# Kernel optimization log

Measured on AMD Instinct MI355X. Metric: run time of the kernel, lower is better.

Reference implementation:

```python
import jax, jax.numpy as jnp
import numpy as np

B, L, HID, NH = 8, 1024, 1024, 16
DH = HID // NH
EPS = 1e-12


def _linear(x, W, b):
    # torch nn.Linear: y = x @ W.T + b
    return jnp.einsum('ble,oe->blo', x, W) + b


def _attend(qx, kx, vx, mask, Wq, bq, Wk, bk, Wv, bv):
    q = _linear(qx, Wq, bq).reshape(B, -1, NH, DH)
    k = _linear(kx, Wk, bk).reshape(B, -1, NH, DH)
    v = _linear(vx, Wv, bv).reshape(B, -1, NH, DH)
    scores = jnp.einsum('bqhd,bkhd->bhqk', q, k) / np.sqrt(DH).astype(np.float32)
    scores = scores + mask  # additive mask broadcast [B,1,1,Lk]
    probs = jax.nn.softmax(scores, axis=-1)  # dropout = identity (eval mode)
    ctx = jnp.einsum('bhqk,bkhd->bqhd', probs, v)
    return ctx.reshape(B, -1, HID)


def _layernorm(x, gamma, beta):
    mu = jnp.mean(x, axis=-1, keepdims=True)
    var = jnp.mean(jnp.square(x - mu), axis=-1, keepdims=True)
    return gamma * (x - mu) * jax.lax.rsqrt(var + EPS) + beta


def setup_inputs():
    key = jax.random.key(0)
    ks = jax.random.split(key, 20)
    s = 0.02
    d = {
        'cinput_tensor': jax.random.normal(ks[0], (B, L, HID), jnp.float32),
        'qinput_tensor': jax.random.normal(ks[1], (B, L, HID), jnp.float32),
        'attention_mask': jnp.zeros((B, 1, 1, L), jnp.float32),
        'qattention_mask': jnp.zeros((B, 1, 1, L), jnp.float32),
    }
    names = ['Wq', 'Wk', 'Wv', 'Wqq', 'Wqk', 'Wqv', 'Wo']
    for i, n in enumerate(names):
        d[n] = jax.random.normal(ks[2 + i], (HID, HID), jnp.float32) * s
        d['b' + n[1:]] = jnp.zeros((HID,), jnp.float32)
    d['gamma'] = jnp.ones((HID,), jnp.float32)
    d['beta'] = jnp.zeros((HID,), jnp.float32)
    return d


def reference(cinput_tensor, qinput_tensor, attention_mask, qattention_mask,
              Wq, bq, Wk, bk, Wv, bv, Wqq, bqq, Wqk, bqk, Wqv, bqv,
              Wo, bo, gamma, beta):
    enc, dec = cinput_tensor, qinput_tensor
    # c-branch: query from dec, key/value from enc
    ctx = _attend(dec, enc, enc, attention_mask, Wq, bq, Wk, bk, Wv, bv)
    # q-branch: query from enc, key/value from dec
    qctx = _attend(enc, dec, dec, qattention_mask, Wqq, bqq, Wqk, bqk, Wqv, bqv)
    # output: same dense/LayerNorm reused, and BOTH residuals add cinput_tensor
    # (faithful to the original module, including its apparent bug)
    c_out = _layernorm(_linear(ctx, Wo, bo) + cinput_tensor, gamma, beta)
    q_out = _layernorm(_linear(qctx, Wo, bo) + cinput_tensor, gamma, beta)
    return (c_out, q_out)
```

## Files before the change

### kernel.cpp

```cpp
#include <hip/hip_runtime.h>

typedef __bf16 bf16;
typedef unsigned short u16;
typedef __bf16 bf16x8 __attribute__((ext_vector_type(8)));
typedef __bf16 bf16x4 __attribute__((ext_vector_type(4)));
typedef float f32x4 __attribute__((ext_vector_type(4)));

#define GLD16(g, l) __builtin_amdgcn_global_load_lds( \
    (const __attribute__((address_space(1))) void*)(g), \
    (__attribute__((address_space(3))) void*)(l), 16, 0, 0)

#define MFMA_BF16 __builtin_amdgcn_mfma_f32_16x16x32_bf16

#define FENCE() asm volatile("" ::: "memory")
#define BARRIER() do { FENCE(); __builtin_amdgcn_s_barrier(); FENCE(); } while (0)

struct CvtFlat { const float* s[9]; bf16* d[9]; int off[10]; };

__global__ __launch_bounds__(256) void cvt_flat(CvtFlat a) {
  const int g = blockIdx.x * 256 + threadIdx.x;
  int seg = 0;
  #pragma unroll
  for (int i = 1; i < 9; ++i) seg += (g >= a.off[i]) ? 1 : 0;
  const int loc = (g - a.off[seg]) * 4;
  const f32x4 v = *(const f32x4*)(a.s[seg] + loc);
  bf16x4 o;
  #pragma unroll
  for (int j = 0; j < 4; ++j) o[j] = (bf16)v[j];
  *(bf16x4*)(a.d[seg] + loc) = o;
}

struct GemmDesc {
  const bf16* X;
  const bf16* W;
  const float* B;
  const float* R;
  bf16* Y;
  int vt;
};
struct GemmArgs { GemmDesc d[6]; };

__global__ __launch_bounds__(256, 2) void gemm128(GemmArgs args) {
  const GemmDesc g = args.d[blockIdx.z];
  __shared__ u16 As[128 * 64];
  __shared__ u16 Bs[128 * 64];
  const int tid = threadIdx.x;
  const int w = tid >> 6, lane = tid & 63;
  const int lq = lane >> 4, ll = lane & 15;
  const int lin = blockIdx.x + (blockIdx.y << 3);
  const int ntile = (lin >> 3) & 7;
  const int mtile = (lin & 7) | ((lin >> 6) << 3);
  const int m0 = mtile * 128, n0 = ntile * 128;
  const int wm = (w >> 1) * 64, wn = (w & 1) * 64;
  f32x4 acc[4][4] = {};

  #pragma unroll
  for (int k0 = 0; k0 < 1024; k0 += 64) {
    #pragma unroll
    for (int i = 0; i < 4; ++i) {
      const int sb = w * 256 + i * 64;
      const int s = sb + lane;
      const int r = s >> 3, c = (s & 7) ^ (r & 7);
      GLD16(g.X + (m0 + r) * 1024 + k0 + c * 8, &As[sb * 8]);
      GLD16(g.W + (n0 + r) * 1024 + k0 + c * 8, &Bs[sb * 8]);
    }
    __syncthreads();
    #pragma unroll
    for (int kk = 0; kk < 64; kk += 32) {
      const int cb = (kk >> 3) + lq;
      bf16x8 a[4], b[4];
      #pragma unroll
      for (int t = 0; t < 4; ++t) {
        const int m = wm + t * 16 + ll;
        a[t] = *(const bf16x8*)&As[m * 64 + ((cb ^ (m & 7)) << 3)];
        const int n = wn + t * 16 + ll;
        b[t] = *(const bf16x8*)&Bs[n * 64 + ((cb ^ (n & 7)) << 3)];
      }
      #pragma unroll
      for (int mt = 0; mt < 4; ++mt)
        #pragma unroll
        for (int nt = 0; nt < 4; ++nt)
          acc[mt][nt] = MFMA_BF16(a[mt], b[nt], acc[mt][nt], 0, 0, 0);
    }
    __syncthreads();
  }

  float biasv[4];
  #pragma unroll
  for (int nt = 0; nt < 4; ++nt) biasv[nt] = g.B[n0 + wn + nt * 16 + ll];

  #pragma unroll
  for (int mt = 0; mt < 4; ++mt) {
    #pragma unroll
    for (int r = 0; r < 4; ++r) {
      const int m = m0 + wm + mt * 16 + lq * 4 + r;
      #pragma unroll
      for (int nt = 0; nt < 4; ++nt) {
        const int n = n0 + wn + nt * 16 + ll;
        float v = acc[mt][nt][r] + biasv[nt];
        if (g.R) v += g.R[m * 1024 + n];
        if (!g.vt) {
          g.Y[m * 1024 + n] = (bf16)v;
        } else {
          const int bb = m >> 10, tok = m & 1023;
          g.Y[(((bb << 4) + (n >> 6)) * 64 + (n & 63)) * 1024 + tok] = (bf16)v;
        }
      }
    }
  }
}

struct AttnDesc { const bf16* Qp; const bf16* Kp; const bf16* Vt; const float* mask; bf16* ctx; };

__global__ __launch_bounds__(256, 4) void attn_kernel(AttnDesc A0, AttnDesc A1) {
  const AttnDesc A = blockIdx.z ? A1 : A0;
  __shared__ u16 Ks[2 * 64 * 64];
  __shared__ u16 Vts[2 * 64 * 64];
  __shared__ u16 Pts[4 * 1024];
  const int tid = threadIdx.x;
  const int w = tid >> 6, lane = tid & 63;
  const int lq = lane >> 4, ll = lane & 15;
  const int lin = blockIdx.x + (blockIdx.y << 3);
  const int bh = (lin & 7) | ((lin >> 6) << 3);
  const int q0 = ((lin >> 3) & 7) * 128;
  const int b = bh >> 4, h = bh & 15;
  const float* mrow = A.mask + b * 1024;

  #pragma unroll
  for (int i = 0; i < 4; ++i) {
    const int sb = w * 256 + i * 64;
    const int s = sb + lane;
    const int r = s >> 3, c = (s & 7) ^ (r & 7);
    GLD16(A.Qp + (b * 1024 + q0 + r) * 1024 + h * 64 + c * 8, &Ks[sb * 8]);
  }
  __syncthreads();
  bf16x8 bq[2][2];
  #pragma unroll
  for (int nt = 0; nt < 2; ++nt)
    #pragma unroll
    for (int kd = 0; kd < 2; ++kd) {
      const int row = w * 32 + nt * 16 + ll;
      const int c8 = kd * 4 + lq;
      bq[nt][kd] = *(const bf16x8*)&Ks[row * 64 + ((c8 ^ (row & 7)) << 3)];
    }
  __syncthreads();

  auto stage_kv = [&](int kt) {
    const int kk0 = kt << 6;
    const int db = (kt & 1) << 12;
    #pragma unroll
    for (int i = 0; i < 2; ++i) {
      const int sb = i * 256 + w * 64;
      const int s = sb + lane;
      const int r = s >> 3, c = (s & 7) ^ (r & 7);
      GLD16(A.Kp + (b * 1024 + kk0 + r) * 1024 + h * 64 + c * 8, &Ks[db + sb * 8]);
      GLD16(A.Vt + ((bh << 6) + r) * 1024 + kk0 + c * 8, &Vts[db + sb * 8]);
    }
  };

  f32x4 oacc[4][2] = {};
  float rsum[2] = {0.f, 0.f};

  stage_kv(0);

  for (int kt = 0; kt < 16; ++kt) {
    const int kk0 = kt << 6;
    const int db = (kt & 1) << 12;
    f32x4 mvk[2][2];
    #pragma unroll
    for (int qtr = 0; qtr < 2; ++qtr)
      #pragma unroll
      for (int mh = 0; mh < 2; ++mh)
        mvk[qtr][mh] = *(const f32x4*)&mrow[kk0 + qtr * 32 + mh * 16 + lq * 4];
    FENCE();
    if (kt < 15) {
      stage_kv(kt + 1);
      asm volatile("s_waitcnt vmcnt(8)" ::: "memory");
    } else {
      asm volatile("s_waitcnt vmcnt(4)" ::: "memory");
    }
    BARRIER();

    #pragma unroll
    for (int qtr = 0; qtr < 2; ++qtr) {
      bf16x8 ak[2][2];
      #pragma unroll
      for (int mh = 0; mh < 2; ++mh) {
        const int row = qtr * 32 + mh * 16 + ll;
        #pragma unroll
        for (int kd = 0; kd < 2; ++kd) {
          const int c8 = kd * 4 + lq;
          ak[mh][kd] = *(const bf16x8*)&Ks[db + row * 64 + ((c8 ^ (row & 7)) << 3)];
        }
      }
      f32x4 sacc[2][2] = {};
      __builtin_amdgcn_s_setprio(1);
      #pragma unroll
      for (int mh = 0; mh < 2; ++mh)
        #pragma unroll
        for (int nt = 0; nt < 2; ++nt)
          #pragma unroll
          for (int kd = 0; kd < 2; ++kd)
            sacc[mh][nt] = MFMA_BF16(ak[mh][kd], bq[nt][kd], sacc[mh][nt], 0, 0, 0);
      __builtin_amdgcn_s_setprio(0);

      #pragma unroll
      for (int mh = 0; mh < 2; ++mh)
        #pragma unroll
        for (int nt = 0; nt < 2; ++nt) {
          bf16x4 pv;
          #pragma unroll
          for (int rr = 0; rr < 4; ++rr) {
            const float p = __expf(fmaf(sacc[mh][nt][rr], 0.125f, mvk[qtr][mh][rr]));
            rsum[nt] += p;
            pv[rr] = (bf16)p;
          }
          const int row = nt * 16 + ll;
          const int gq = mh * 2 + (lq >> 1);
          *(bf16x4*)&Pts[w * 1024 + row * 32 + ((gq ^ (row & 3)) << 3) + (lq & 1) * 4] = pv;
        }

      bf16x8 bp[2];
      #pragma unroll
      for (int nt = 0; nt < 2; ++nt) {
        const int row = nt * 16 + ll;
        bp[nt] = *(const bf16x8*)&Pts[w * 1024 + row * 32 + ((lq ^ (row & 3)) << 3)];
      }
      __builtin_amdgcn_s_setprio(1);
      #pragma unroll
      for (int mtd = 0; mtd < 4; ++mtd) {
        const int row = mtd * 16 + ll;
        const int c8v = ((qtr << 2) + lq) ^ (row & 7);
        const bf16x8 av = *(const bf16x8*)&Vts[db + row * 64 + (c8v << 3)];
        oacc[mtd][0] = MFMA_BF16(av, bp[0], oacc[mtd][0], 0, 0, 0);
        oacc[mtd][1] = MFMA_BF16(av, bp[1], oacc[mtd][1], 0, 0, 0);
      }
      __builtin_amdgcn_s_setprio(0);
    }
    BARRIER();
  }

  #pragma unroll
  for (int nt = 0; nt < 2; ++nt) {
    rsum[nt] += __shfl_xor(rsum[nt], 16, 64);
    rsum[nt] += __shfl_xor(rsum[nt], 32, 64);
  }

  #pragma unroll
  for (int nt = 0; nt < 2; ++nt) {
    const float inv = 1.f / rsum[nt];
    const int tok = q0 + w * 32 + nt * 16 + ll;
    #pragma unroll
    for (int mtd = 0; mtd < 4; ++mtd) {
      bf16x4 ov;
      #pragma unroll
      for (int rr = 0; rr < 4; ++rr) ov[rr] = (bf16)(oacc[mtd][nt][rr] * inv);
      *(bf16x4*)&A.ctx[(size_t)(b * 1024 + tok) * 1024 + h * 64 + mtd * 16 + lq * 4] = ov;
    }
  }
}

__global__ __launch_bounds__(256) void ln_kernel(const bf16* __restrict__ pre_c,
                                                 const bf16* __restrict__ pre_q,
                                                 const float* __restrict__ gamma,
                                                 const float* __restrict__ beta,
                                                 float* __restrict__ out) {
  const int row = blockIdx.x;
  const bf16* src = (row < 8192) ? (pre_c + (size_t)row * 1024)
                                 : (pre_q + (size_t)(row - 8192) * 1024);
  float* dst = out + (size_t)row * 1024;
  const int t = threadIdx.x;
  const bf16x4 xv = *(const bf16x4*)(src + t * 4);
  float x[4]; float s = 0.f, ss = 0.f;
  #pragma unroll
  for (int i = 0; i < 4; ++i) { x[i] = (float)xv[i]; s += x[i]; ss += x[i] * x[i]; }
  #pragma unroll
  for (int off = 1; off < 64; off <<= 1) { s += __shfl_xor(s, off, 64); ss += __shfl_xor(ss, off, 64); }
  __shared__ float red[8];
  const int w = t >> 6, lane = t & 63;
  if (lane == 0) { red[w * 2] = s; red[w * 2 + 1] = ss; }
  __syncthreads();
  s  = red[0] + red[2] + red[4] + red[6];
  ss = red[1] + red[3] + red[5] + red[7];
  const float mu = s * (1.f / 1024.f);
  float var = ss * (1.f / 1024.f) - mu * mu;
  var = fmaxf(var, 0.f);
  const float rs = rsqrtf(var + 1e-12f);
  const f32x4 gv = *(const f32x4*)(gamma + t * 4);
  const f32x4 bv = *(const f32x4*)(beta + t * 4);
  f32x4 yv;
  #pragma unroll
  for (int i = 0; i < 4; ++i) yv[i] = gv[i] * (x[i] - mu) * rs + bv[i];
  *(f32x4*)(dst + t * 4) = yv;
}

extern "C" void kernel_launch(void* const* d_in, const int* in_sizes, int n_in,
                              void* d_out, int out_size, void* d_ws, size_t ws_size,
                              hipStream_t stream) {
  const float* enc    = (const float*)d_in[0];
  const float* dec    = (const float*)d_in[1];
  const float* mask_c = (const float*)d_in[2];
  const float* mask_q = (const float*)d_in[3];
  const float* Wq  = (const float*)d_in[4];  const float* bq  = (const float*)d_in[5];
  const float* Wk  = (const float*)d_in[6];  const float* bk  = (const float*)d_in[7];
  const float* Wv  = (const float*)d_in[8];  const float* bv  = (const float*)d_in[9];
  const float* Wqq = (const float*)d_in[10]; const float* bqq = (const float*)d_in[11];
  const float* Wqk = (const float*)d_in[12]; const float* bqk = (const float*)d_in[13];
  const float* Wqv = (const float*)d_in[14]; const float* bqv = (const float*)d_in[15];
  const float* Wo  = (const float*)d_in[16]; const float* bo  = (const float*)d_in[17];
  const float* gamma = (const float*)d_in[18];
  const float* beta  = (const float*)d_in[19];
  float* out = (float*)d_out;

  bf16* ws = (bf16*)d_ws;
  const size_t XSZ = (size_t)8192 * 1024;
  const size_t WSZ = (size_t)1024 * 1024;
  bf16* enc_b = ws;
  bf16* dec_b = enc_b + XSZ;
  bf16* Wb[7];
  for (int i = 0; i < 7; ++i) Wb[i] = dec_b + XSZ + i * WSZ;
  bf16* after_w = Wb[6] + WSZ;

  CvtFlat ca;
  ca.s[0] = enc; ca.d[0] = enc_b;
  ca.s[1] = dec; ca.d[1] = dec_b;
  const float* Wsrc[7] = {Wq, Wk, Wv, Wqq, Wqk, Wqv, Wo};
  for (int i = 0; i < 7; ++i) { ca.s[2 + i] = Wsrc[i]; ca.d[2 + i] = Wb[i]; }
  int running = 0;
  const int segn[9] = {(int)(XSZ / 4), (int)(XSZ / 4), (int)(WSZ / 4), (int)(WSZ / 4),
                       (int)(WSZ / 4), (int)(WSZ / 4), (int)(WSZ / 4), (int)(WSZ / 4), (int)(WSZ / 4)};
  for (int i = 0; i < 9; ++i) { ca.off[i] = running; running += segn[i]; }
  ca.off[9] = running;
  const int cvt_blocks = running / 256;

  const size_t need_par = (size_t)(23 + 48) * 1024 * 1024 * 2;

  cvt_flat<<<dim3(cvt_blocks), 256, 0, stream>>>(ca);

  if (ws_size >= need_par) {
    bf16* Qc  = after_w;        bf16* Kc  = Qc + XSZ;  bf16* Vtc = Kc + XSZ;
    bf16* Qq  = Vtc + XSZ;      bf16* Kq  = Qq + XSZ;  bf16* Vtq = Kq + XSZ;
    bf16* ctx_c = enc_b;
    bf16* ctx_q = dec_b;
    bf16* pre_c = Qc;
    bf16* pre_q = Qq;

    GemmArgs pa = {};
    pa.d[0] = {dec_b, Wb[0], bq,  nullptr, Qc,  0};
    pa.d[1] = {enc_b, Wb[1], bk,  nullptr, Kc,  0};
    pa.d[2] = {enc_b, Wb[2], bv,  nullptr, Vtc, 1};
    pa.d[3] = {enc_b, Wb[3], bqq, nullptr, Qq,  0};
    pa.d[4] = {dec_b, Wb[4], bqk, nullptr, Kq,  0};
    pa.d[5] = {dec_b, Wb[5], bqv, nullptr, Vtq, 1};
    gemm128<<<dim3(8, 64, 6), 256, 0, stream>>>(pa);

    AttnDesc a0 = {Qc, Kc, Vtc, mask_c, ctx_c};
    AttnDesc a1 = {Qq, Kq, Vtq, mask_q, ctx_q};
    attn_kernel<<<dim3(8, 128, 2), 256, 0, stream>>>(a0, a1);

    GemmArgs oa = {};
    oa.d[0] = {ctx_c, Wb[6], bo, enc, pre_c, 0};
    oa.d[1] = {ctx_q, Wb[6], bo, enc, pre_q, 0};
    gemm128<<<dim3(8, 64, 2), 256, 0, stream>>>(oa);

    ln_kernel<<<dim3(16384), 256, 0, stream>>>(pre_c, pre_q, gamma, beta, out);
  } else {
    bf16* Q  = after_w;  bf16* K = Q + XSZ;  bf16* Vt = K + XSZ;
    bf16* ctx_c = Vt + XSZ;
    bf16* ctx_q = ctx_c + XSZ;
    bf16* pre_c = Q;
    bf16* pre_q = K;

    GemmArgs pa = {};
    pa.d[0] = {dec_b, Wb[0], bq,  nullptr, Q,  0};
    pa.d[1] = {enc_b, Wb[1], bk,  nullptr, K,  0};
    pa.d[2] = {enc_b, Wb[2], bv,  nullptr, Vt, 1};
    gemm128<<<dim3(8, 64, 3), 256, 0, stream>>>(pa);

    AttnDesc a0 = {Q, K, Vt, mask_c, ctx_c};
    attn_kernel<<<dim3(8, 128, 1), 256, 0, stream>>>(a0, a0);

    GemmArgs pb = {};
    pb.d[0] = {enc_b, Wb[3], bqq, nullptr, Q,  0};
    pb.d[1] = {dec_b, Wb[4], bqk, nullptr, K,  0};
    pb.d[2] = {dec_b, Wb[5], bqv, nullptr, Vt, 1};
    gemm128<<<dim3(8, 64, 3), 256, 0, stream>>>(pb);

    AttnDesc a1 = {Q, K, Vt, mask_q, ctx_q};
    attn_kernel<<<dim3(8, 128, 1), 256, 0, stream>>>(a1, a1);

    GemmArgs oa = {};
    oa.d[0] = {ctx_c, Wb[6], bo, enc, pre_c, 0};
    oa.d[1] = {ctx_q, Wb[6], bo, enc, pre_q, 0};
    gemm128<<<dim3(8, 64, 2), 256, 0, stream>>>(oa);

    ln_kernel<<<dim3(16384), 256, 0, stream>>>(pre_c, pre_q, gamma, beta, out);
  }
}
```

Before: 471.0 us.

## Double-buffer LDS tiles in gemm128 to overlap global loads with MFMA

The GEMM kernel now keeps two LDS buffers for the A and B tiles. It issues the next k-tile's global-to-LDS loads before computing on the current tile, and uses an explicit vmcnt wait so only the older loads must complete. This aims to hide global memory latency behind the MFMA work instead of stalling at a full sync every iteration. LDS use doubles to 64KB per block, which may limit the two-blocks-per-CU occupancy target, and the k loop is no longer fully unrolled.

```diff
diff --git a/kernel.cpp b/kernel.cpp
--- a/kernel.cpp
+++ b/kernel.cpp
@@ -1,4 +1,5 @@
 #include <hip/hip_runtime.h>
+
 
 typedef __bf16 bf16;
 typedef unsigned short u16;
@@ -42,8 +43,8 @@
 
 __global__ __launch_bounds__(256, 2) void gemm128(GemmArgs args) {
   const GemmDesc g = args.d[blockIdx.z];
-  __shared__ u16 As[128 * 64];
-  __shared__ u16 Bs[128 * 64];
+  __shared__ u16 As[2][8192];
+  __shared__ u16 Bs[2][8192];
   const int tid = threadIdx.x;
   const int w = tid >> 6, lane = tid & 63;
   const int lq = lane >> 4, ll = lane & 15;
@@ -54,17 +55,38 @@
   const int wm = (w >> 1) * 64, wn = (w & 1) * 64;
   f32x4 acc[4][4] = {};
 
-  #pragma unroll
-  for (int k0 = 0; k0 < 1024; k0 += 64) {
+  int aoff[4], boff[4], sdst[4];
+  #pragma unroll
+  for (int i = 0; i < 4; ++i) {
+    const int sb = w * 256 + i * 64;
+    const int s = sb + lane;
+    const int r = s >> 3, c = (s & 7) ^ (r & 7);
+    aoff[i] = (m0 + r) * 1024 + c * 8;
+    boff[i] = (n0 + r) * 1024 + c * 8;
+    sdst[i] = sb * 8;
+  }
+
+  auto stage = [&](int k, int buf) {
+    const int k0 = k << 6;
     #pragma unroll
     for (int i = 0; i < 4; ++i) {
-      const int sb = w * 256 + i * 64;
-      const int s = sb + lane;
-      const int r = s >> 3, c = (s & 7) ^ (r & 7);
-      GLD16(g.X + (m0 + r) * 1024 + k0 + c * 8, &As[sb * 8]);
-      GLD16(g.W + (n0 + r) * 1024 + k0 + c * 8, &Bs[sb * 8]);
-    }
-    __syncthreads();
+      GLD16(g.X + aoff[i] + k0, &As[buf][sdst[i]]);
+      GLD16(g.W + boff[i] + k0, &Bs[buf][sdst[i]]);
+    }
+  };
+
+  stage(0, 0);
+
+  for (int k = 0; k < 16; ++k) {
+    const int buf = k & 1;
+    if (k < 15) {
+      stage(k + 1, buf ^ 1);
+      asm volatile("s_waitcnt vmcnt(8)" ::: "memory");
+    } else {
+      asm volatile("s_waitcnt vmcnt(0)" ::: "memory");
+    }
+    BARRIER();
+
     #pragma unroll
     for (int kk = 0; kk < 64; kk += 32) {
       const int cb = (kk >> 3) + lq;
@@ -72,9 +94,9 @@
       #pragma unroll
       for (int t = 0; t < 4; ++t) {
         const int m = wm + t * 16 + ll;
-        a[t] = *(const bf16x8*)&As[m * 64 + ((cb ^ (m & 7)) << 3)];
+        a[t] = *(const bf16x8*)&As[buf][m * 64 + ((cb ^ (m & 7)) << 3)];
         const int n = wn + t * 16 + ll;
-        b[t] = *(const bf16x8*)&Bs[n * 64 + ((cb ^ (n & 7)) << 3)];
+        b[t] = *(const bf16x8*)&Bs[buf][n * 64 + ((cb ^ (n & 7)) << 3)];
       }
       #pragma unroll
       for (int mt = 0; mt < 4; ++mt)
@@ -82,7 +104,7 @@
         for (int nt = 0; nt < 4; ++nt)
           acc[mt][nt] = MFMA_BF16(a[mt], b[nt], acc[mt][nt], 0, 0, 0);
     }
-    __syncthreads();
+    BARRIER();
   }
 
   float biasv[4];
```

Measured after the change: 509.1 us. 1.08x slower.
